# Optimization experiments

Measured on AMD Instinct MI355X. Metric: run time of the kernel, lower is better.

## Reference

```python
import jax, jax.numpy as jnp
import numpy as np

NL, H, D, DK, DFF = 6, 12, 384, 32, 1536
VOCAB, MAXPOS, B, L = 30522, 512, 64, 512
LN_EPS = 1e-12


def layer_norm(x, g, b):
    m = jnp.mean(x, axis=-1, keepdims=True)
    v = jnp.mean((x - m) ** 2, axis=-1, keepdims=True)
    return (x - m) * jax.lax.rsqrt(v + LN_EPS) * g + b


def _l2norm(t):
    return t / (jnp.linalg.norm(t, axis=-1, keepdims=True) + 1e-6)


def delta_layer(x, mask, Wq, bq, Wk, bk, Wv, bv, Wb, gf_logit, gs_logit, Wo, bo):
    # Hierarchical DeltaNet: delta-rule linear attention with fast & slow decaying states.
    Bb, Ll, _ = x.shape
    q = _l2norm((x @ Wq + bq).reshape(Bb, Ll, H, DK))
    k = _l2norm((x @ Wk + bk).reshape(Bb, Ll, H, DK))
    v = (x @ Wv + bv).reshape(Bb, Ll, H, DK)
    beta = jax.nn.sigmoid(x @ Wb)  # [B,L,H] per-head write strength
    k = k * mask[:, :, None, None]
    beta = beta * mask[:, :, None]
    gf = jax.nn.sigmoid(gf_logit)[None, :, None, None]  # fast decay ~0.3
    gs = jax.nn.sigmoid(gs_logit)[None, :, None, None]  # slow decay ~0.85

    xs = (jnp.moveaxis(q, 1, 0), jnp.moveaxis(k, 1, 0),
          jnp.moveaxis(v, 1, 0), jnp.moveaxis(beta, 1, 0))

    def step(carry, inp):
        Sf, Ss = carry  # each [B,H,DK,DK]
        qt, kt, vt, bt = inp
        pf = jnp.einsum('bhk,bhkv->bhv', kt, Sf)
        ps = jnp.einsum('bhk,bhkv->bhv', kt, Ss)
        Sf = gf * Sf + jnp.einsum('bhk,bhv->bhkv', kt, bt[..., None] * (vt - pf))
        Ss = gs * Ss + jnp.einsum('bhk,bhv->bhkv', kt, bt[..., None] * (vt - ps))
        ot = 0.5 * (jnp.einsum('bhk,bhkv->bhv', qt, Sf)
                    + jnp.einsum('bhk,bhkv->bhv', qt, Ss))
        return (Sf, Ss), ot

    S0 = jnp.zeros((Bb, H, DK, DK), x.dtype)
    _, o = jax.lax.scan(step, (S0, S0), xs)  # o: [L,B,H,DK]
    o = jnp.moveaxis(o, 0, 1).reshape(Bb, Ll, D)
    return o @ Wo + bo


def setup_inputs():
    key = jax.random.key(0)
    ks = jax.random.split(key, 16)
    r = lambda i, shape: jax.random.normal(ks[i], shape, jnp.float32) * 0.02
    lf = float(np.log(0.3 / 0.7))
    ls = float(np.log(0.85 / 0.15))
    return {
        'input_ids': jax.random.randint(ks[0], (B, L), 0, VOCAB),
        'attention_mask': jnp.ones((B, L), jnp.float32),
        'word_emb': r(1, (VOCAB, D)),
        'pos_emb': r(2, (MAXPOS, D)),
        'type_emb': r(3, (1, D)),
        'emb_ln_g': jnp.ones((D,)), 'emb_ln_b': jnp.zeros((D,)),
        'Wq': r(4, (NL, D, D)), 'bq': jnp.zeros((NL, D)),
        'Wk': r(5, (NL, D, D)), 'bk': jnp.zeros((NL, D)),
        'Wv': r(6, (NL, D, D)), 'bv': jnp.zeros((NL, D)),
        'Wb': r(7, (NL, D, H)),
        'decay_fast': jnp.full((NL, H), lf, jnp.float32),
        'decay_slow': jnp.full((NL, H), ls, jnp.float32),
        'Wo': r(8, (NL, D, D)), 'bo': jnp.zeros((NL, D)),
        'ln1_g': jnp.ones((NL, D)), 'ln1_b': jnp.zeros((NL, D)),
        'W1': r(9, (NL, D, DFF)), 'b1': jnp.zeros((NL, DFF)),
        'W2': r(10, (NL, DFF, D)), 'b2': jnp.zeros((NL, D)),
        'ln2_g': jnp.ones((NL, D)), 'ln2_b': jnp.zeros((NL, D)),
    }


def reference(input_ids, attention_mask, word_emb, pos_emb, type_emb,
              emb_ln_g, emb_ln_b, Wq, bq, Wk, bk, Wv, bv, Wb,
              decay_fast, decay_slow, Wo, bo, ln1_g, ln1_b,
              W1, b1, W2, b2, ln2_g, ln2_b):
    Ll = input_ids.shape[1]
    x = word_emb[input_ids] + pos_emb[None, :Ll] + type_emb[0]
    x = layer_norm(x, emb_ln_g, emb_ln_b)
    for i in range(NL):
        a = delta_layer(x, attention_mask, Wq[i], bq[i], Wk[i], bk[i],
                        Wv[i], bv[i], Wb[i], decay_fast[i], decay_slow[i],
                        Wo[i], bo[i])
        x = layer_norm(x + a, ln1_g[i], ln1_b[i])
        h = jax.nn.gelu(x @ W1[i] + b1[i])  # BertIntermediate (dense+gelu)
        h = jax.nn.gelu(h)                  # extra F.gelu in forward (as written)
        h = h @ W2[i] + b2[i]
        x = layer_norm(x + h, ln2_g[i], ln2_b[i])
    m = attention_mask[..., None]
    emb = jnp.sum(x * m, axis=1) / jnp.clip(jnp.sum(m, axis=1), 1e-9)
    n = jnp.clip(jnp.linalg.norm(emb, axis=1, keepdims=True), 1e-12)
    return emb / n
```

## Files before the change

### kernel.cpp

```cpp
#include <hip/hip_runtime.h>
#include <cstdint>
#include <cstddef>
#include <cmath>

#define NLAYER 6
#define NH 12
#define DMODEL 384
#define DHEAD 32
#define DFFN 1536
#define BATCH 64
#define SEQ 512
#define NROWS (BATCH*SEQ)
#define DQKV 1152

typedef unsigned short ushort;
typedef __attribute__((ext_vector_type(8))) short bf16x8;
typedef __attribute__((ext_vector_type(4))) float f32x4;


__device__ inline float bf2f(ushort u) {
    union { unsigned int i; float f; } c; c.i = ((unsigned int)u) << 16; return c.f;
}
__device__ inline ushort f2bf(float f) {
    union { float f; unsigned int i; } c; c.f = f;
    unsigned int i = c.i;
    unsigned int lsb = (i >> 16) & 1u;
    i += 0x7fffu + lsb;
    return (ushort)(i >> 16);
}

__device__ inline float wave_reduce_sum(float v) {
    #pragma unroll
    for (int m = 32; m >= 1; m >>= 1) v += __shfl_xor(v, m, 64);
    return v;
}

__device__ inline float sigmoidf(float x) { return 1.0f / (1.0f + expf(-x)); }

__device__ inline float gelu_tanh(float x) {
    const float c = 0.7978845608028654f;
    float y = c * (x + 0.044715f * x * x * x);
    float e = __expf(2.0f * y);
    float t = 1.0f - 2.0f * __builtin_amdgcn_rcpf(e + 1.0f);
    return 0.5f * x * (1.0f + t);
}

__device__ inline void async16(const ushort* g, ushort* l) {
    __builtin_amdgcn_global_load_lds(
        (const __attribute__((address_space(1))) unsigned int*)g,
        (__attribute__((address_space(3))) unsigned int*)l,
        16, 0, 0);
}

__global__ __launch_bounds__(256)
void convT_kernel(const float* __restrict__ W, ushort* __restrict__ WT, int K, int N,
                  size_t lStride, int nOff)
{
    __shared__ float t[32][33];
    int k0 = blockIdx.x * 32, n0 = blockIdx.y * 32, L = blockIdx.z;
    const float* Wl = W + (size_t)L * K * N;
    ushort* WTl = WT + (size_t)L * lStride;
    int tx = threadIdx.x & 31, ty = threadIdx.x >> 5;
    #pragma unroll
    for (int i = 0; i < 4; ++i)
        t[ty + 8 * i][tx] = Wl[(size_t)(k0 + ty + 8 * i) * N + n0 + tx];
    __syncthreads();
    #pragma unroll
    for (int i = 0; i < 4; ++i)
        WTl[(size_t)(nOff + n0 + ty + 8 * i) * K + k0 + tx] = f2bf(t[tx][ty + 8 * i]);
}

__global__ __launch_bounds__(384)
void biascat_kernel(const float* __restrict__ bq, const float* __restrict__ bk,
                    const float* __restrict__ bv, float* __restrict__ dst)
{
    int L = blockIdx.x, d = threadIdx.x;
    dst[(size_t)L * DQKV + d]             = bq[(size_t)L * DMODEL + d];
    dst[(size_t)L * DQKV + DMODEL + d]    = bk[(size_t)L * DMODEL + d];
    dst[(size_t)L * DQKV + 2*DMODEL + d]  = bv[(size_t)L * DMODEL + d];
}

__global__ __launch_bounds__(256)
void embed_ln_kernel(const int* __restrict__ ids, const float* __restrict__ we,
                     const float* __restrict__ pe, const float* __restrict__ te,
                     const float* __restrict__ g, const float* __restrict__ bb,
                     float* __restrict__ x, ushort* __restrict__ xb)
{
    int row = blockIdx.x * 4 + (threadIdx.x >> 6);
    int lane = threadIdx.x & 63;
    int l = row & (SEQ - 1);
    int id = ids[row];
    float vals[6];
    float s = 0.f;
    #pragma unroll
    for (int t = 0; t < 6; ++t) {
        int d = lane + 64 * t;
        float v = we[(size_t)id * DMODEL + d] + pe[(size_t)l * DMODEL + d] + te[d];
        vals[t] = v; s += v;
    }
    s = wave_reduce_sum(s);
    float m = s * (1.0f / DMODEL);
    float s2 = 0.f;
    #pragma unroll
    for (int t = 0; t < 6; ++t) { float dd = vals[t] - m; s2 += dd * dd; }
    s2 = wave_reduce_sum(s2);
    float rs = rsqrtf(s2 * (1.0f / DMODEL) + 1e-12f);
    #pragma unroll
    for (int t = 0; t < 6; ++t) {
        int d = lane + 64 * t;
        float val = (vals[t] - m) * rs * g[d] + bb[d];
        x[(size_t)row * DMODEL + d] = val;
        xb[(size_t)row * DMODEL + d] = f2bf(val);
    }
}

__global__ __launch_bounds__(256)
void add_ln_kernel(float* x, ushort* __restrict__ xb, const ushort* __restrict__ r,
                   const float* __restrict__ g, const float* __restrict__ bb)
{
    int row = blockIdx.x * 4 + (threadIdx.x >> 6);
    int lane = threadIdx.x & 63;
    float vals[6];
    float s = 0.f;
    #pragma unroll
    for (int t = 0; t < 6; ++t) {
        int d = lane + 64 * t;
        size_t idx = (size_t)row * DMODEL + d;
        float v = x[idx] + bf2f(r[idx]);
        vals[t] = v; s += v;
    }
    s = wave_reduce_sum(s);
    float m = s * (1.0f / DMODEL);
    float s2 = 0.f;
    #pragma unroll
    for (int t = 0; t < 6; ++t) { float dd = vals[t] - m; s2 += dd * dd; }
    s2 = wave_reduce_sum(s2);
    float rs = rsqrtf(s2 * (1.0f / DMODEL) + 1e-12f);
    #pragma unroll
    for (int t = 0; t < 6; ++t) {
        int d = lane + 64 * t;
        size_t idx = (size_t)row * DMODEL + d;
        float val = (vals[t] - m) * rs * g[d] + bb[d];
        x[idx] = val;
        xb[idx] = f2bf(val);
    }
}

__global__ __launch_bounds__(256)
void add_ln_ip_kernel(float* x, ushort* xb,
                      const float* __restrict__ g, const float* __restrict__ bb)
{
    int row = blockIdx.x * 4 + (threadIdx.x >> 6);
    int lane = threadIdx.x & 63;
    float vals[6];
    float s = 0.f;
    #pragma unroll
    for (int t = 0; t < 6; ++t) {
        int d = lane + 64 * t;
        size_t idx = (size_t)row * DMODEL + d;
        float v = x[idx] + bf2f(xb[idx]);
        vals[t] = v; s += v;
    }
    s = wave_reduce_sum(s);
    float m = s * (1.0f / DMODEL);
    float s2 = 0.f;
    #pragma unroll
    for (int t = 0; t < 6; ++t) { float dd = vals[t] - m; s2 += dd * dd; }
    s2 = wave_reduce_sum(s2);
    float rs = rsqrtf(s2 * (1.0f / DMODEL) + 1e-12f);
    #pragma unroll
    for (int t = 0; t < 6; ++t) {
        int d = lane + 64 * t;
        size_t idx = (size_t)row * DMODEL + d;
        float val = (vals[t] - m) * rs * g[d] + bb[d];
        x[idx] = val;
        xb[idx] = f2bf(val);
    }
}

template<typename TC>
__global__ __launch_bounds__(256)
void gemm_mfma(const ushort* __restrict__ A, const ushort* __restrict__ WT,
               const float* __restrict__ bias, TC* __restrict__ C,
               int M, int N, int K, int Astride, int act)
{
    __shared__ __align__(16) ushort As[128 * 64];
    __shared__ __align__(16) ushort Bs[128 * 64];
    int tid = threadIdx.x;
    int lane = tid & 63, wv = tid >> 6;
    int waveM = wv >> 1, waveN = wv & 1;
    int lm = lane & 15, quad = lane >> 4;

    int bid = blockIdx.x + gridDim.x * blockIdx.y;
    int nwg = gridDim.x * gridDim.y;
    int w = bid;
    if ((nwg & 7) == 0) {
        int cpx = nwg >> 3;
        w = (bid & 7) * cpx + (bid >> 3);
    }
    int xt = w / gridDim.y;
    int yt = w % gridDim.y;
    int row0 = xt * 128, col0 = yt * 128;

    int srow = lane >> 3, sseg = lane & 7;

    f32x4 acc[4][4] = {};

    for (int k0 = 0; k0 < K; k0 += 64) {
        __syncthreads();
        #pragma unroll
        for (int i = 0; i < 4; ++i) {
            int r = wv * 32 + i * 8 + srow;
            int sg = sseg ^ (r & 7);
            async16(A  + (size_t)(row0 + r) * Astride + k0 + sg * 8, &As[(wv * 32 + i * 8) * 64]);
            async16(WT + (size_t)(col0 + r) * K + k0 + sg * 8, &Bs[(wv * 32 + i * 8) * 64]);
        }
        __syncthreads();

        #pragma unroll
        for (int ks = 0; ks < 2; ++ks) {
            int physA = ((ks * 4 + quad) ^ (lm & 7)) * 8;
            bf16x8 af[4], bf[4];
            #pragma unroll
            for (int mt = 0; mt < 4; ++mt)
                af[mt] = *(const bf16x8*)&As[(waveM * 64 + mt * 16 + lm) * 64 + physA];
            #pragma unroll
            for (int nt = 0; nt < 4; ++nt)
                bf[nt] = *(const bf16x8*)&Bs[(waveN * 64 + nt * 16 + lm) * 64 + physA];
            #pragma unroll
            for (int mt = 0; mt < 4; ++mt)
                #pragma unroll
                for (int nt = 0; nt < 4; ++nt)
                    acc[mt][nt] = __builtin_amdgcn_mfma_f32_16x16x32_bf16(af[mt], bf[nt], acc[mt][nt], 0, 0, 0);
        }
    }

    #pragma unroll
    for (int mt = 0; mt < 4; ++mt) {
        #pragma unroll
        for (int nt = 0; nt < 4; ++nt) {
            int col = col0 + waveN * 64 + nt * 16 + lm;
            float bv = bias[col];
            #pragma unroll
            for (int r = 0; r < 4; ++r) {
                int row = row0 + waveM * 64 + mt * 16 + quad * 4 + r;
                float val = acc[mt][nt][r] + bv;
                if (act == 1) val = gelu_tanh(gelu_tanh(val));
                if constexpr (sizeof(TC) == 2)
                    C[(size_t)row * N + col] = f2bf(val);
                else
                    C[(size_t)row * N + col] = val;
            }
        }
    }
}

__global__ __launch_bounds__(256)
void beta_kernel(const ushort* __restrict__ xb, const float* __restrict__ Wb,
                 const float* __restrict__ mask, float* __restrict__ beta)
{
    int row = blockIdx.x * 4 + (threadIdx.x >> 6);
    int lane = threadIdx.x & 63;
    float xr[6];
    #pragma unroll
    for (int t = 0; t < 6; ++t) xr[t] = bf2f(xb[(size_t)row * DMODEL + lane + 64 * t]);
    float mine = 0.f;
    #pragma unroll
    for (int h = 0; h < NH; ++h) {
        float p = 0.f;
        #pragma unroll
        for (int t = 0; t < 6; ++t) p += xr[t] * Wb[(size_t)(lane + 64 * t) * NH + h];
        p = wave_reduce_sum(p);
        if (lane == h) mine = p;
    }
    if (lane < NH) beta[(size_t)row * NH + lane] = sigmoidf(mine) * mask[row];
}

#define SCAN_T 32
#define SPAD 36
__global__ __launch_bounds__(64)
void scan_kernel(const ushort* __restrict__ qkv, const float* __restrict__ beta,
                 const float* __restrict__ mask,
                 const float* __restrict__ dfast, const float* __restrict__ dslow,
                 ushort* __restrict__ o)
{
    __shared__ __align__(16) float qs[2][SCAN_T][SPAD];
    __shared__ __align__(16) float ks[2][SCAN_T][SPAD];
    __shared__ __align__(16) float vs[2][SCAN_T][SPAD];
    __shared__ float bs[2][SCAN_T];

    int gw = blockIdx.x;
    int lane = threadIdx.x;
    int half = lane >> 5, n = lane & 31;
    int bh = gw * 2 + half;
    int myb = bh / NH, myh = bh % NH;

    float gf = sigmoidf(dfast[myh]);
    float gsl = sigmoidf(dslow[myh]);
    float2 gf2 = make_float2(gf, gf), gs2 = make_float2(gsl, gsl);
    float2 Sf[16], Ss[16];
    #pragma unroll
    for (int j = 0; j < 16; ++j) { Sf[j] = make_float2(0.f, 0.f); Ss[j] = make_float2(0.f, 0.f); }

    uint4 pq[4], pk[4], pv[4];
    float pb, pmk;
    {
        size_t ra = (size_t)(myb * SEQ + n) * DQKV + myh * DHEAD;
        #pragma unroll
        for (int s = 0; s < 4; ++s) {
            pq[s] = *(const uint4*)(qkv + ra + s * 8);
            pk[s] = *(const uint4*)(qkv + ra + DMODEL + s * 8);
            pv[s] = *(const uint4*)(qkv + ra + 2 * DMODEL + s * 8);
        }
        pb  = beta[(size_t)(myb * SEQ + n) * NH + myh];
        pmk = mask[myb * SEQ + n];
    }

    for (int t0 = 0; t0 < SEQ; t0 += SCAN_T) {
        __syncthreads();
        {
            ushort tq[32], tk[32], tv[32];
            #pragma unroll
            for (int s = 0; s < 4; ++s) {
                *(uint4*)(tq + s * 8) = pq[s];
                *(uint4*)(tk + s * 8) = pk[s];
                *(uint4*)(tv + s * 8) = pv[s];
            }
            float qv[32], kv[32];
            float sq = 0.f, sk = 0.f;
            #pragma unroll
            for (int j = 0; j < 32; ++j) {
                qv[j] = bf2f(tq[j]); sq += qv[j] * qv[j];
                kv[j] = bf2f(tk[j]); sk += kv[j] * kv[j];
            }
            float rq = 1.0f / (sqrtf(sq) + 1e-6f);
            float rk = pmk / (sqrtf(sk) + 1e-6f);
            #pragma unroll
            for (int s = 0; s < 8; ++s) {
                float4 fq, fk, fv;
                fq.x = qv[s*4+0]*rq; fq.y = qv[s*4+1]*rq; fq.z = qv[s*4+2]*rq; fq.w = qv[s*4+3]*rq;
                fk.x = kv[s*4+0]*rk; fk.y = kv[s*4+1]*rk; fk.z = kv[s*4+2]*rk; fk.w = kv[s*4+3]*rk;
                fv.x = bf2f(tv[s*4+0]); fv.y = bf2f(tv[s*4+1]); fv.z = bf2f(tv[s*4+2]); fv.w = bf2f(tv[s*4+3]);
                *(float4*)&qs[half][n][s * 4] = fq;
                *(float4*)&ks[half][n][s * 4] = fk;
                *(float4*)&vs[half][n][s * 4] = fv;
            }
            bs[half][n] = pb;
        }
        __syncthreads();

        if (t0 + SCAN_T < SEQ) {
            size_t ra = (size_t)(myb * SEQ + t0 + SCAN_T + n) * DQKV + myh * DHEAD;
            #pragma unroll
            for (int s = 0; s < 4; ++s) {
                pq[s] = *(const uint4*)(qkv + ra + s * 8);
                pk[s] = *(const uint4*)(qkv + ra + DMODEL + s * 8);
                pv[s] = *(const uint4*)(qkv + ra + 2 * DMODEL + s * 8);
            }
            pb  = beta[(size_t)(myb * SEQ + t0 + SCAN_T + n) * NH + myh];
            pmk = mask[myb * SEQ + t0 + SCAN_T + n];
        }

        #pragma unroll 4
        for (int t = 0; t < SCAN_T; ++t) {
            float2 kt[16], qt[16];
            #pragma unroll
            for (int s = 0; s < 8; ++s) {
                *(float4*)&kt[s * 2] = *(const float4*)&ks[half][t][s * 4];
                *(float4*)&qt[s * 2] = *(const float4*)&qs[half][t][s * 4];
            }
            float vt = vs[half][t][n], bt = bs[half][t];

            float2 pf0 = kt[0] * Sf[0], pf1 = kt[1] * Sf[1], pf2 = kt[2] * Sf[2], pf3 = kt[3] * Sf[3];
            float2 ps0 = kt[0] * Ss[0], ps1 = kt[1] * Ss[1], ps2 = kt[2] * Ss[2], ps3 = kt[3] * Ss[3];
            #pragma unroll
            for (int j = 4; j < 16; j += 4) {
                pf0 += kt[j] * Sf[j];     pf1 += kt[j + 1] * Sf[j + 1];
                pf2 += kt[j + 2] * Sf[j + 2]; pf3 += kt[j + 3] * Sf[j + 3];
                ps0 += kt[j] * Ss[j];     ps1 += kt[j + 1] * Ss[j + 1];
                ps2 += kt[j + 2] * Ss[j + 2]; ps3 += kt[j + 3] * Ss[j + 3];
            }
            float2 pfv = (pf0 + pf1) + (pf2 + pf3);
            float2 psv = (ps0 + ps1) + (ps2 + ps3);
            float pft = pfv.x + pfv.y, pst = psv.x + psv.y;

            float cf = bt * (vt - pft), cs = bt * (vt - pst);
            float2 cf2 = make_float2(cf, cf), cs2 = make_float2(cs, cs);

            float2 o0 = make_float2(0.f, 0.f), o1 = o0, o2 = o0, o3 = o0;
            #pragma unroll
            for (int j = 0; j < 16; j += 4) {
                Sf[j] = gf2 * Sf[j] + kt[j] * cf2;         Ss[j] = gs2 * Ss[j] + kt[j] * cs2;
                Sf[j+1] = gf2 * Sf[j+1] + kt[j+1] * cf2;   Ss[j+1] = gs2 * Ss[j+1] + kt[j+1] * cs2;
                Sf[j+2] = gf2 * Sf[j+2] + kt[j+2] * cf2;   Ss[j+2] = gs2 * Ss[j+2] + kt[j+2] * cs2;
                Sf[j+3] = gf2 * Sf[j+3] + kt[j+3] * cf2;   Ss[j+3] = gs2 * Ss[j+3] + kt[j+3] * cs2;
                o0 += qt[j] * (Sf[j] + Ss[j]);
                o1 += qt[j+1] * (Sf[j+1] + Ss[j+1]);
                o2 += qt[j+2] * (Sf[j+2] + Ss[j+2]);
                o3 += qt[j+3] * (Sf[j+3] + Ss[j+3]);
            }
            float2 ov = (o0 + o1) + (o2 + o3);
            float ott = ov.x + ov.y;
            o[((size_t)(myb * SEQ + t0 + t)) * DQKV + myh * DHEAD + n] = f2bf(0.5f * ott);
        }
    }
}

__global__ __launch_bounds__(384)
void pool_kernel(const float* __restrict__ x, const float* __restrict__ mask,
                 float* __restrict__ out)
{
    int b = blockIdx.x;
    int d = threadIdx.x;
    float acc = 0.f, msum = 0.f;
    for (int l = 0; l < SEQ; ++l) {
        float mk = mask[b * SEQ + l];
        acc += x[((size_t)b * SEQ + l) * DMODEL + d] * mk;
        msum += mk;
    }
    float emb = acc / fmaxf(msum, 1e-9f);
    __shared__ float red[6];
    float ss = wave_reduce_sum(emb * emb);
    int wvi = d >> 6, ln = d & 63;
    if (ln == 0) red[wvi] = ss;
    __syncthreads();
    float tot = 0.f;
    #pragma unroll
    for (int i = 0; i < 6; ++i) tot += red[i];
    float nrm = fmaxf(sqrtf(tot), 1e-12f);
    out[(size_t)b * DMODEL + d] = emb / nrm;
}


extern "C" void kernel_launch(void* const* d_in, const int* in_sizes, int n_in,
                              void* d_out, int out_size, void* d_ws, size_t ws_size,
                              hipStream_t stream)
{
    const int*   ids   = (const int*)d_in[0];
    const float* mask  = (const float*)d_in[1];
    const float* we    = (const float*)d_in[2];
    const float* pe    = (const float*)d_in[3];
    const float* te    = (const float*)d_in[4];
    const float* elg   = (const float*)d_in[5];
    const float* elb   = (const float*)d_in[6];
    const float* Wq    = (const float*)d_in[7];
    const float* bq    = (const float*)d_in[8];
    const float* Wk    = (const float*)d_in[9];
    const float* bk    = (const float*)d_in[10];
    const float* Wv    = (const float*)d_in[11];
    const float* bv    = (const float*)d_in[12];
    const float* Wb    = (const float*)d_in[13];
    const float* dfast = (const float*)d_in[14];
    const float* dslow = (const float*)d_in[15];
    const float* Wo    = (const float*)d_in[16];
    const float* bo    = (const float*)d_in[17];
    const float* l1g   = (const float*)d_in[18];
    const float* l1b   = (const float*)d_in[19];
    const float* W1    = (const float*)d_in[20];
    const float* b1    = (const float*)d_in[21];
    const float* W2    = (const float*)d_in[22];
    const float* b2    = (const float*)d_in[23];
    const float* l2g   = (const float*)d_in[24];
    const float* l2b   = (const float*)d_in[25];
    float* out = (float*)d_out;

    const size_t RD = (size_t)NROWS * DMODEL;
    float* x      = (float*)d_ws;
    float* betab  = x + RD;
    ushort* xb    = (ushort*)(betab + (size_t)NROWS * NH);
    ushort* qkvb  = xb + RD;
    ushort* ab    = qkvb + (size_t)NROWS * DQKV;
    ushort* WqkvT = ab + RD;
    ushort* WoT   = WqkvT + (size_t)NLAYER * DQKV * DMODEL;
    ushort* W1T   = WoT + (size_t)NLAYER * DMODEL * DMODEL;
    ushort* W2T   = W1T + (size_t)NLAYER * DMODEL * DFFN;
    float* biasqkv = (float*)(W2T + (size_t)NLAYER * DFFN * DMODEL);

    dim3 blk256(256);
    dim3 rowsGrid(NROWS / 4);
    dim3 gemmGrid_QKV(NROWS / 128, DQKV / 128);
    dim3 gemmGrid_D(NROWS / 128, DMODEL / 128);
    dim3 gemmGrid_F1(NROWS / 128, DFFN / 128);
    dim3 gemmGrid_F2(NROWS / 128, DMODEL / 128);
    dim3 scanGrid(BATCH * NH / 2);

    const size_t lsQKV = (size_t)DQKV * DMODEL;
    convT_kernel<<<dim3(12, 12, NLAYER), blk256, 0, stream>>>(Wq, WqkvT, DMODEL, DMODEL, lsQKV, 0);
    convT_kernel<<<dim3(12, 12, NLAYER), blk256, 0, stream>>>(Wk, WqkvT, DMODEL, DMODEL, lsQKV, DMODEL);
    convT_kernel<<<dim3(12, 12, NLAYER), blk256, 0, stream>>>(Wv, WqkvT, DMODEL, DMODEL, lsQKV, 2*DMODEL);
    convT_kernel<<<dim3(12, 12, NLAYER), blk256, 0, stream>>>(Wo, WoT, DMODEL, DMODEL, (size_t)DMODEL*DMODEL, 0);
    convT_kernel<<<dim3(12, 48, NLAYER), blk256, 0, stream>>>(W1, W1T, DMODEL, DFFN, (size_t)DMODEL*DFFN, 0);
    convT_kernel<<<dim3(48, 12, NLAYER), blk256, 0, stream>>>(W2, W2T, DFFN, DMODEL, (size_t)DFFN*DMODEL, 0);
    biascat_kernel<<<dim3(NLAYER), dim3(384), 0, stream>>>(bq, bk, bv, biasqkv);

    embed_ln_kernel<<<rowsGrid, blk256, 0, stream>>>(ids, we, pe, te, elg, elb, x, xb);

    for (int i = 0; i < NLAYER; ++i) {
        const ushort* WqkvT_i = WqkvT + (size_t)i * lsQKV;
        const ushort* WoT_i   = WoT + (size_t)i * DMODEL * DMODEL;
        const float*  Wb_i    = Wb  + (size_t)i * DMODEL * NH;
        const ushort* W1T_i   = W1T + (size_t)i * DMODEL * DFFN;
        const ushort* W2T_i   = W2T + (size_t)i * DFFN * DMODEL;

        gemm_mfma<ushort><<<gemmGrid_QKV, blk256, 0, stream>>>(xb, WqkvT_i, biasqkv + (size_t)i * DQKV,
                                                               qkvb, NROWS, DQKV, DMODEL, DMODEL, 0);
        beta_kernel<<<rowsGrid, blk256, 0, stream>>>(xb, Wb_i, mask, betab);
        scan_kernel<<<scanGrid, dim3(64), 0, stream>>>(qkvb, betab, mask,
                                                       dfast + i * NH, dslow + i * NH, qkvb);
        gemm_mfma<ushort><<<gemmGrid_D, blk256, 0, stream>>>(qkvb, WoT_i, bo + i * DMODEL, ab,
                                                             NROWS, DMODEL, DMODEL, DQKV, 0);
        add_ln_kernel<<<rowsGrid, blk256, 0, stream>>>(x, xb, ab, l1g + i * DMODEL, l1b + i * DMODEL);

        {
            ushort* hbuf = qkvb;
            gemm_mfma<ushort><<<gemmGrid_F1, blk256, 0, stream>>>(xb, W1T_i, b1 + i * DFFN, hbuf,
                                                                  NROWS, DFFN, DMODEL, DMODEL, 1);
            gemm_mfma<ushort><<<gemmGrid_F2, blk256, 0, stream>>>(hbuf, W2T_i, b2 + i * DMODEL, xb,
                                                                  NROWS, DMODEL, DFFN, DFFN, 0);
            add_ln_ip_kernel<<<rowsGrid, blk256, 0, stream>>>(x, xb, l2g + i * DMODEL, l2b + i * DMODEL);
        }
    }

    pool_kernel<<<dim3(BATCH), dim3(384), 0, stream>>>(x, mask, out);
}
```

Measured before the change: 3.017 ms.

## Split fast and slow delta states across wave halves in scan kernel

The scan kernel now handles one (batch, head) pair per 64-lane block instead of two. One half of the wave carries the fast-decay state and the other the slow-decay state, so each thread holds 16 float2 of state instead of 32 and does half the per-step arithmetic. Each half loads and normalises half of the q/k/v vector, and the L2 norms are combined with a cross-half shuffle. Per-step outputs are summed through a small LDS buffer, and the grid doubles to BATCH*NH blocks. This shortens the serial per-step critical path and raises parallelism, at the cost of extra LDS traffic and an LDS exchange on every step.

```diff
diff --git a/kernel.cpp b/kernel.cpp
--- a/kernel.cpp
+++ b/kernel.cpp
@@ -52,6 +52,16 @@
         16, 0, 0);
 }
 
+__device__ inline float dot16(const float2* a, const float2* b) {
+    float2 s0 = a[0]*b[0], s1 = a[1]*b[1], s2 = a[2]*b[2], s3 = a[3]*b[3];
+    #pragma unroll
+    for (int j = 4; j < 16; j += 4) {
+        s0 += a[j]*b[j]; s1 += a[j+1]*b[j+1]; s2 += a[j+2]*b[j+2]; s3 += a[j+3]*b[j+3];
+    }
+    float2 s = (s0 + s1) + (s2 + s3);
+    return s.x + s.y;
+}
+
 __global__ __launch_bounds__(256)
 void convT_kernel(const float* __restrict__ W, ushort* __restrict__ WT, int K, int N,
                   size_t lStride, int nOff)
@@ -284,34 +294,31 @@
                  const float* __restrict__ dfast, const float* __restrict__ dslow,
                  ushort* __restrict__ o)
 {
-    __shared__ __align__(16) float qs[2][SCAN_T][SPAD];
-    __shared__ __align__(16) float ks[2][SCAN_T][SPAD];
-    __shared__ __align__(16) float vs[2][SCAN_T][SPAD];
-    __shared__ float bs[2][SCAN_T];
-
-    int gw = blockIdx.x;
+    __shared__ __align__(16) float qs[SCAN_T][SPAD];
+    __shared__ __align__(16) float ks[SCAN_T][SPAD];
+    __shared__ __align__(16) float vs[SCAN_T][SPAD];
+    __shared__ float bs[SCAN_T];
+    __shared__ float osb[64];
+
+    int bh = blockIdx.x;
     int lane = threadIdx.x;
     int half = lane >> 5, n = lane & 31;
-    int bh = gw * 2 + half;
+    int h16 = half << 4;
     int myb = bh / NH, myh = bh % NH;
 
-    float gf = sigmoidf(dfast[myh]);
-    float gsl = sigmoidf(dslow[myh]);
-    float2 gf2 = make_float2(gf, gf), gs2 = make_float2(gsl, gsl);
-    float2 Sf[16], Ss[16];
-    #pragma unroll
-    for (int j = 0; j < 16; ++j) { Sf[j] = make_float2(0.f, 0.f); Ss[j] = make_float2(0.f, 0.f); }
-
-    uint4 pq[4], pk[4], pv[4];
+    float g = sigmoidf(half ? dslow[myh] : dfast[myh]);
+    float2 g2 = make_float2(g, g);
+    float2 S[16];
+    #pragma unroll
+    for (int j = 0; j < 16; ++j) S[j] = make_float2(0.f, 0.f);
+
+    uint4 pq[2], pk[2], pv[2];
     float pb, pmk;
     {
-        size_t ra = (size_t)(myb * SEQ + n) * DQKV + myh * DHEAD;
-        #pragma unroll
-        for (int s = 0; s < 4; ++s) {
-            pq[s] = *(const uint4*)(qkv + ra + s * 8);
-            pk[s] = *(const uint4*)(qkv + ra + DMODEL + s * 8);
-            pv[s] = *(const uint4*)(qkv + ra + 2 * DMODEL + s * 8);
-        }
+        size_t ra = (size_t)(myb * SEQ + n) * DQKV + myh * DHEAD + h16;
+        pq[0] = *(const uint4*)(qkv + ra);     pq[1] = *(const uint4*)(qkv + ra + 8);
+        pk[0] = *(const uint4*)(qkv + ra + DMODEL);     pk[1] = *(const uint4*)(qkv + ra + DMODEL + 8);
+        pv[0] = *(const uint4*)(qkv + ra + 2*DMODEL);   pv[1] = *(const uint4*)(qkv + ra + 2*DMODEL + 8);
         pb  = beta[(size_t)(myb * SEQ + n) * NH + myh];
         pmk = mask[myb * SEQ + n];
     }
@@ -319,44 +326,40 @@
     for (int t0 = 0; t0 < SEQ; t0 += SCAN_T) {
         __syncthreads();
         {
-            ushort tq[32], tk[32], tv[32];
-            #pragma unroll
-            for (int s = 0; s < 4; ++s) {
-                *(uint4*)(tq + s * 8) = pq[s];
-                *(uint4*)(tk + s * 8) = pk[s];
-                *(uint4*)(tv + s * 8) = pv[s];
-            }
-            float qv[32], kv[32];
+            ushort tq[16], tk[16], tv[16];
+            *(uint4*)tq = pq[0]; *(uint4*)(tq + 8) = pq[1];
+            *(uint4*)tk = pk[0]; *(uint4*)(tk + 8) = pk[1];
+            *(uint4*)tv = pv[0]; *(uint4*)(tv + 8) = pv[1];
+            float qv[16], kv[16];
             float sq = 0.f, sk = 0.f;
             #pragma unroll
-            for (int j = 0; j < 32; ++j) {
+            for (int j = 0; j < 16; ++j) {
                 qv[j] = bf2f(tq[j]); sq += qv[j] * qv[j];
                 kv[j] = bf2f(tk[j]); sk += kv[j] * kv[j];
             }
+            sq += __shfl_xor(sq, 32, 64);
+            sk += __shfl_xor(sk, 32, 64);
             float rq = 1.0f / (sqrtf(sq) + 1e-6f);
             float rk = pmk / (sqrtf(sk) + 1e-6f);
             #pragma unroll
-            for (int s = 0; s < 8; ++s) {
+            for (int s2 = 0; s2 < 4; ++s2) {
                 float4 fq, fk, fv;
-                fq.x = qv[s*4+0]*rq; fq.y = qv[s*4+1]*rq; fq.z = qv[s*4+2]*rq; fq.w = qv[s*4+3]*rq;
-                fk.x = kv[s*4+0]*rk; fk.y = kv[s*4+1]*rk; fk.z = kv[s*4+2]*rk; fk.w = kv[s*4+3]*rk;
-                fv.x = bf2f(tv[s*4+0]); fv.y = bf2f(tv[s*4+1]); fv.z = bf2f(tv[s*4+2]); fv.w = bf2f(tv[s*4+3]);
-                *(float4*)&qs[half][n][s * 4] = fq;
-                *(float4*)&ks[half][n][s * 4] = fk;
-                *(float4*)&vs[half][n][s * 4] = fv;
+                fq.x = qv[s2*4+0]*rq; fq.y = qv[s2*4+1]*rq; fq.z = qv[s2*4+2]*rq; fq.w = qv[s2*4+3]*rq;
+                fk.x = kv[s2*4+0]*rk; fk.y = kv[s2*4+1]*rk; fk.z = kv[s2*4+2]*rk; fk.w = kv[s2*4+3]*rk;
+                fv.x = bf2f(tv[s2*4+0]); fv.y = bf2f(tv[s2*4+1]); fv.z = bf2f(tv[s2*4+2]); fv.w = bf2f(tv[s2*4+3]);
+                *(float4*)&qs[n][h16 + s2*4] = fq;
+                *(float4*)&ks[n][h16 + s2*4] = fk;
+                *(float4*)&vs[n][h16 + s2*4] = fv;
             }
-            bs[half][n] = pb;
+            if (!half) bs[n] = pb;
         }
         __syncthreads();
 
         if (t0 + SCAN_T < SEQ) {
-            size_t ra = (size_t)(myb * SEQ + t0 + SCAN_T + n) * DQKV + myh * DHEAD;
-            #pragma unroll
-            for (int s = 0; s < 4; ++s) {
-                pq[s] = *(const uint4*)(qkv + ra + s * 8);
-                pk[s] = *(const uint4*)(qkv + ra + DMODEL + s * 8);
-                pv[s] = *(const uint4*)(qkv + ra + 2 * DMODEL + s * 8);
-            }
+            size_t ra = (size_t)(myb * SEQ + t0 + SCAN_T + n) * DQKV + myh * DHEAD + h16;
+            pq[0] = *(const uint4*)(qkv + ra);     pq[1] = *(const uint4*)(qkv + ra + 8);
+            pk[0] = *(const uint4*)(qkv + ra + DMODEL);     pk[1] = *(const uint4*)(qkv + ra + DMODEL + 8);
+            pv[0] = *(const uint4*)(qkv + ra + 2*DMODEL);   pv[1] = *(const uint4*)(qkv + ra + 2*DMODEL + 8);
             pb  = beta[(size_t)(myb * SEQ + t0 + SCAN_T + n) * NH + myh];
             pmk = mask[myb * SEQ + t0 + SCAN_T + n];
         }
@@ -365,43 +368,35 @@
         for (int t = 0; t < SCAN_T; ++t) {
             float2 kt[16], qt[16];
             #pragma unroll
-            for (int s = 0; s < 8; ++s) {
-                *(float4*)&kt[s * 2] = *(const float4*)&ks[half][t][s * 4];
-                *(float4*)&qt[s * 2] = *(const float4*)&qs[half][t][s * 4];
+            for (int s2 = 0; s2 < 8; ++s2) {
+                *(float4*)&kt[s2 * 2] = *(const float4*)&ks[t][s2 * 4];
+                *(float4*)&qt[s2 * 2] = *(const float4*)&qs[t][s2 * 4];
             }
-            float vt = vs[half][t][n], bt = bs[half][t];
-
-            float2 pf0 = kt[0] * Sf[0], pf1 = kt[1] * Sf[1], pf2 = kt[2] * Sf[2], pf3 = kt[3] * Sf[3];
-            float2 ps0 = kt[0] * Ss[0], ps1 = kt[1] * Ss[1], ps2 = kt[2] * Ss[2], ps3 = kt[3] * Ss[3];
-            #pragma unroll
-            for (int j = 4; j < 16; j += 4) {
-                pf0 += kt[j] * Sf[j];     pf1 += kt[j + 1] * Sf[j + 1];
-                pf2 += kt[j + 2] * Sf[j + 2]; pf3 += kt[j + 3] * Sf[j + 3];
-                ps0 += kt[j] * Ss[j];     ps1 += kt[j + 1] * Ss[j + 1];
-                ps2 += kt[j + 2] * Ss[j + 2]; ps3 += kt[j + 3] * Ss[j + 3];
-            }
-            float2 pfv = (pf0 + pf1) + (pf2 + pf3);
-            float2 psv = (ps0 + ps1) + (ps2 + ps3);
-            float pft = pfv.x + pfv.y, pst = psv.x + psv.y;
-
-            float cf = bt * (vt - pft), cs = bt * (vt - pst);
-            float2 cf2 = make_float2(cf, cf), cs2 = make_float2(cs, cs);
+            float vt = vs[t][n], bt = bs[t];
+
+            float p = dot16(kt, S);
+            float c = bt * (vt - p);
+            float2 c2 = make_float2(c, c);
 
             float2 o0 = make_float2(0.f, 0.f), o1 = o0, o2 = o0, o3 = o0;
             #pragma unroll
             for (int j = 0; j < 16; j += 4) {
-                Sf[j] = gf2 * Sf[j] + kt[j] * cf2;         Ss[j] = gs2 * Ss[j] + kt[j] * cs2;
-                Sf[j+1] = gf2 * Sf[j+1] + kt[j+1] * cf2;   Ss[j+1] = gs2 * Ss[j+1] + kt[j+1] * cs2;
-                Sf[j+2] = gf2 * Sf[j+2] + kt[j+2] * cf2;   Ss[j+2] = gs2 * Ss[j+2] + kt[j+2] * cs2;
-                Sf[j+3] = gf2 * Sf[j+3] + kt[j+3] * cf2;   Ss[j+3] = gs2 * Ss[j+3] + kt[j+3] * cs2;
-                o0 += qt[j] * (Sf[j] + Ss[j]);
-                o1 += qt[j+1] * (Sf[j+1] + Ss[j+1]);
-                o2 += qt[j+2] * (Sf[j+2] + Ss[j+2]);
-                o3 += qt[j+3] * (Sf[j+3] + Ss[j+3]);
+                S[j]   = g2 * S[j]   + kt[j]   * c2;
+                S[j+1] = g2 * S[j+1] + kt[j+1] * c2;
+                S[j+2] = g2 * S[j+2] + kt[j+2] * c2;
+                S[j+3] = g2 * S[j+3] + kt[j+3] * c2;
+                o0 += qt[j]   * S[j];
+                o1 += qt[j+1] * S[j+1];
+                o2 += qt[j+2] * S[j+2];
+                o3 += qt[j+3] * S[j+3];
             }
             float2 ov = (o0 + o1) + (o2 + o3);
-            float ott = ov.x + ov.y;
-            o[((size_t)(myb * SEQ + t0 + t)) * DQKV + myh * DHEAD + n] = f2bf(0.5f * ott);
+            float oh = ov.x + ov.y;
+
+            osb[lane] = oh;
+            float osum = osb[n] + osb[n + 32];
+            if (lane < 32)
+                o[((size_t)(myb * SEQ + t0 + t)) * DQKV + myh * DHEAD + n] = f2bf(0.5f * osum);
         }
     }
 }
@@ -482,7 +477,7 @@
     dim3 gemmGrid_D(NROWS / 128, DMODEL / 128);
     dim3 gemmGrid_F1(NROWS / 128, DFFN / 128);
     dim3 gemmGrid_F2(NROWS / 128, DMODEL / 128);
-    dim3 scanGrid(BATCH * NH / 2);
+    dim3 scanGrid(BATCH * NH);
 
     const size_t lsQKV = (size_t)DQKV * DMODEL;
     convT_kernel<<<dim3(12, 12, NLAYER), blk256, 0, stream>>>(Wq, WqkvT, DMODEL, DMODEL, lsQKV, 0);
```

After: 2.797 ms. -7.3%, faster.
